# Performance work log

Measured on AMD Instinct MI355X. Metric: run time of the kernel, lower is better.

The kernel has to match this reference:

```python
import jax, jax.numpy as jnp
import numpy as np

D = 15            # tree depth; leaves at level 0, root at level D
INPUT_DIM = 64
MEM_DIM = 256     # must equal 4*INPUT_DIM (h-update mixes rr with x)
HID_DIM = 128


def _lin(key, fi, fo):
    kw, kb = jax.random.split(key)
    w = jax.random.normal(kw, (fi, fo), jnp.float32) / np.sqrt(fi)
    b = jax.random.normal(kb, (fo,), jnp.float32) * 0.01
    return w, b


def setup_inputs() -> dict:
    key = jax.random.key(0)
    N = 2 ** (D + 1) - 1          # 65535 nodes (complete binary tree, heap order)
    I = 2 ** D - 1                # internal nodes
    depth = np.floor(np.log2(np.arange(1, N + 1))).astype(np.int64)  # depth of node i
    node_order_np = D - depth     # leaves -> 0, root -> D
    parents = np.repeat(np.arange(I, dtype=np.int64), 2)   # sorted, consecutive per parent
    children = np.arange(1, N, dtype=np.int64)             # heap children 2i+1, 2i+2
    adjacency_list = jnp.asarray(np.stack([parents, children], axis=1))
    edge_order = jnp.asarray(node_order_np[parents])
    ks = jax.random.split(key, 24)
    inp = {
        'oper_feat': jax.random.uniform(ks[0], (N, 4), jnp.float32),
        'tb_feat': jax.random.uniform(ks[1], (N, 11), jnp.float32),
        'filter_feat': jax.random.uniform(ks[2], (N, 18), jnp.float32),
        'join_feat': jax.random.uniform(ks[3], (N, 37), jnp.float32),
        'c_a': jax.random.normal(ks[4], (N, MEM_DIM), jnp.float32) * 0.1,
        'c_b': jax.random.normal(ks[5], (N, 5 * INPUT_DIM), jnp.float32) * 0.1,
    }
    inp['w_op1'], inp['b_op1'] = _lin(ks[6], 4, INPUT_DIM)
    inp['w_op2'], inp['b_op2'] = _lin(ks[7], INPUT_DIM, INPUT_DIM)
    inp['w_tb1'], inp['b_tb1'] = _lin(ks[8], 11, INPUT_DIM)
    inp['w_tb2'], inp['b_tb2'] = _lin(ks[9], INPUT_DIM, INPUT_DIM)
    inp['w_ft1'], inp['b_ft1'] = _lin(ks[10], 18, INPUT_DIM)
    inp['w_ft2'], inp['b_ft2'] = _lin(ks[11], INPUT_DIM, INPUT_DIM)
    inp['w_jn1'], inp['b_jn1'] = _lin(ks[12], 37, INPUT_DIM)
    inp['w_jn2'], inp['b_jn2'] = _lin(ks[13], INPUT_DIM, INPUT_DIM)
    inp['w_xou'], inp['b_xou'] = _lin(ks[14], 4 * INPUT_DIM, 3 * MEM_DIM)
    inp['w_ab'], inp['b_ab'] = _lin(ks[15], MEM_DIM, MEM_DIM)
    inp['w_btoa'], inp['b_btoa'] = _lin(ks[16], 5 * INPUT_DIM, MEM_DIM)
    inp['w_ca'], inp['b_ca'] = _lin(ks[17], 4 * INPUT_DIM, MEM_DIM)
    inp['w_cb'], inp['b_cb'] = _lin(ks[18], 4 * INPUT_DIM, MEM_DIM)
    inp['w_o1'], inp['b_o1'] = _lin(ks[19], MEM_DIM, HID_DIM)
    inp['w_o2'], inp['b_o2'] = _lin(ks[20], HID_DIM, 1)
    inp['node_order'] = jnp.asarray(node_order_np)
    inp['adjacency_list'] = adjacency_list
    inp['edge_order'] = edge_order
    inp['feed'] = 0
    return inp


def _mlp2(f, w1, b1, w2, b2):
    return jax.nn.relu(jax.nn.relu(f @ w1 + b1) @ w2 + b2)


def reference(oper_feat, tb_feat, filter_feat, join_feat, c_a, c_b,
              w_op1, b_op1, w_op2, b_op2, w_tb1, b_tb1, w_tb2, b_tb2,
              w_ft1, b_ft1, w_ft2, b_ft2, w_jn1, b_jn1, w_jn2, b_jn2,
              w_xou, b_xou, w_ab, b_ab, w_btoa, b_btoa, w_ca, b_ca,
              w_cb, b_cb, w_o1, b_o1, w_o2, b_o2,
              node_order, adjacency_list, edge_order, feed):
    N = node_order.shape[0]
    op = _mlp2(oper_feat, w_op1, b_op1, w_op2, b_op2)
    tb = _mlp2(tb_feat, w_tb1, b_tb1, w_tb2, b_tb2)
    ft = _mlp2(filter_feat, w_ft1, b_ft1, w_ft2, b_ft2)
    jn = _mlp2(join_feat, w_jn1, b_jn1, w_jn2, b_jn2)
    x = jnp.concatenate([op, tb, ft, jn], axis=1)        # [N, 4*input_dim] == [N, mem_dim]
    xou = x @ w_xou + b_xou                               # [N, 3*mem_dim]
    xx, ff, rr = jnp.split(xou, 3, axis=1)
    ff = jax.nn.sigmoid(ff)
    rr = jax.nn.sigmoid(rr)
    cb = c_b @ w_btoa + b_btoa                            # con_mpl_btoa (no activation)
    wa = jax.nn.sigmoid(c_a @ w_ca + b_ca)
    wb = jax.nn.sigmoid(cb @ w_cb + b_cb)
    c_ab = jax.nn.relu((wa * c_a + wb * cb) @ w_ab + b_ab)
    c = jnp.zeros((N, MEM_DIM), x.dtype)
    h = jnp.zeros((N, MEM_DIM), x.dtype)
    c = jnp.where((node_order == 0)[:, None], c_a, c)
    c = jnp.where((node_order == feed)[:, None], c_ab, c)
    par = adjacency_list[:, 0]
    chi = adjacency_list[:, 1]
    L = int(node_order.max())
    for n in range(feed + 1, L + 1):
        em = (edge_order == n).astype(x.dtype)[:, None]
        # segment-sum children cell states into their parents (level-n edges only)
        c_sum = jax.ops.segment_sum(c[chi] * em, par, num_segments=N)
        nm = (node_order == n)[:, None]
        c = jnp.where(nm, ff * c_sum + (1.0 - ff) * xx, c)
        h = jnp.where(nm, rr * jnp.tanh(c) + (1.0 - rr) * x, h)
    hid = jax.nn.relu(h @ w_o1 + b_o1)
    return jax.nn.sigmoid(hid @ w_o2 + b_o2)              # [N, 1]
```

## Files before the change

kernel.cpp:

```cpp
#include <hip/hip_runtime.h>
#include <cstdint>

#define I_NODES 32767
#define N_NODES 65535
#define NLEAF   32768

typedef float f32x4 __attribute__((ext_vector_type(4)));
typedef short bf16x8 __attribute__((ext_vector_type(8)));
typedef int   i32x4 __attribute__((ext_vector_type(4)));

__device__ __forceinline__ float sigmoidf_(float v) {
    return 1.0f / (1.0f + __expf(-v));
}
__device__ __forceinline__ short f2bf(float f) {
    union { float f; unsigned u; } v; v.f = f;
    unsigned r = (v.u + 0x7FFF + ((v.u >> 16) & 1)) >> 16;
    return (short)r;
}
__device__ __forceinline__ float bf2f(short b) {
    union { float f; unsigned u; } v; v.u = ((unsigned)(unsigned short)b) << 16;
    return v.f;
}

__global__ __launch_bounds__(256) void encode_kernel(
    const float* __restrict__ oper, const float* __restrict__ tbf,
    const float* __restrict__ ftf,  const float* __restrict__ jnf,
    const float* __restrict__ w_op1, const float* __restrict__ b_op1,
    const float* __restrict__ w_op2, const float* __restrict__ b_op2,
    const float* __restrict__ w_tb1, const float* __restrict__ b_tb1,
    const float* __restrict__ w_tb2, const float* __restrict__ b_tb2,
    const float* __restrict__ w_ft1, const float* __restrict__ b_ft1,
    const float* __restrict__ w_ft2, const float* __restrict__ b_ft2,
    const float* __restrict__ w_jn1, const float* __restrict__ b_jn1,
    const float* __restrict__ w_jn2, const float* __restrict__ b_jn2,
    short* __restrict__ x_out)
{
    __shared__ float w1[70 * 64];
    __shared__ float w2s[64 * 64];
    __shared__ float b1[256], b2[256];
    __shared__ float feat[16][72];
    __shared__ float h1[16][256];

    const int tid = threadIdx.x;

    for (int idx = tid; idx < 70 * 64; idx += 256) {
        int r = idx >> 6, cc = idx & 63;
        float v;
        if (r < 4)       v = w_op1[r * 64 + cc];
        else if (r < 15) v = w_tb1[(r - 4) * 64 + cc];
        else if (r < 33) v = w_ft1[(r - 15) * 64 + cc];
        else             v = w_jn1[(r - 33) * 64 + cc];
        w1[idx] = v;
    }
    {
        int s = tid >> 6, jj = tid & 63;
        b1[tid] = (s == 0) ? b_op1[jj] : (s == 1) ? b_tb1[jj] : (s == 2) ? b_ft1[jj] : b_jn1[jj];
        b2[tid] = (s == 0) ? b_op2[jj] : (s == 1) ? b_tb2[jj] : (s == 2) ? b_ft2[jj] : b_jn2[jj];
    }

    const int node0 = blockIdx.x * 16;
    for (int idx = tid; idx < 16 * 70; idx += 256) {
        int nb = idx / 70, f = idx % 70;
        int node = node0 + nb;
        float v = 0.0f;
        if (node < I_NODES) {
            if (f < 4)       v = oper[node * 4 + f];
            else if (f < 15) v = tbf[node * 11 + (f - 4)];
            else if (f < 33) v = ftf[node * 18 + (f - 15)];
            else             v = jnf[node * 37 + (f - 33)];
        }
        feat[nb][f] = v;
    }
    __syncthreads();

    {
        int j = tid;
        int s = j >> 6, jj = j & 63;
        int off = (s == 0) ? 0 : (s == 1) ? 4 : (s == 2) ? 15 : 33;
        int Ks  = (s == 0) ? 4 : (s == 1) ? 11 : (s == 2) ? 18 : 37;
        for (int nb = 0; nb < 16; nb++) {
            float acc = b1[j];
            for (int k = 0; k < Ks; k++)
                acc += feat[nb][off + k] * w1[(off + k) * 64 + jj];
            h1[nb][j] = fmaxf(acc, 0.0f);
        }
    }
    __syncthreads();

    for (int s = 0; s < 4; s++) {
        const float* w2g = (s == 0) ? w_op2 : (s == 1) ? w_tb2 : (s == 2) ? w_ft2 : w_jn2;
        for (int idx = tid; idx < 4096; idx += 256) w2s[idx] = w2g[idx];
        __syncthreads();
        for (int it = 0; it < 4; it++) {
            int wi = it * 256 + tid;
            int nb = wi >> 6, jj = wi & 63;
            float acc = b2[s * 64 + jj];
            for (int k = 0; k < 64; k++)
                acc += h1[nb][s * 64 + k] * w2s[k * 64 + jj];
            int node = node0 + nb;
            x_out[(size_t)node * 256 + s * 64 + jj] =
                (node < I_NODES) ? f2bf(fmaxf(acc, 0.0f)) : (short)0;
        }
        __syncthreads();
    }
}

template <int ACT, int MODE>
__global__ __launch_bounds__(256) void gemm_mfma(
    const short* __restrict__ A, const short* __restrict__ Bt,
    const float* __restrict__ bias,
    float* __restrict__ fout0, float* __restrict__ fout1, float* __restrict__ fout2,
    short* __restrict__ bout,
    int M, int K, int Nn)
{
    __shared__ short Asl[128 * 40];
    __shared__ short Bsl[128 * 40];

    const int tid = threadIdx.x;
    const int bm = blockIdx.x * 128;
    const int bn = blockIdx.y * 128;
    const int wave = tid >> 6, lane = tid & 63;
    const int m = lane & 15, q = lane >> 4;
    const int rw = (wave & 1) * 64, cw = (wave >> 1) * 64;

    f32x4 acc[4][4] = {};

    for (int k0 = 0; k0 < K; k0 += 32) {
#pragma unroll
        for (int i = 0; i < 2; i++) {
            int id = tid + i * 256;
            int row = id >> 2, ch = id & 3;
            i32x4 va = *(const i32x4*)(A + (size_t)(bm + row) * K + k0 + ch * 8);
            *(i32x4*)&Asl[row * 40 + ch * 8] = va;
            i32x4 vb = *(const i32x4*)(Bt + (size_t)(bn + row) * K + k0 + ch * 8);
            *(i32x4*)&Bsl[row * 40 + ch * 8] = vb;
        }
        __syncthreads();

        bf16x8 bfrag[4];
#pragma unroll
        for (int ct = 0; ct < 4; ct++)
            bfrag[ct] = *(const bf16x8*)&Bsl[(cw + ct * 16 + m) * 40 + q * 8];
#pragma unroll
        for (int rt = 0; rt < 4; rt++) {
            bf16x8 afrag = *(const bf16x8*)&Asl[(rw + rt * 16 + m) * 40 + q * 8];
#pragma unroll
            for (int ct = 0; ct < 4; ct++)
                acc[rt][ct] = __builtin_amdgcn_mfma_f32_16x16x32_bf16(
                    afrag, bfrag[ct], acc[rt][ct], 0, 0, 0);
        }
        __syncthreads();
    }

#pragma unroll
    for (int rt = 0; rt < 4; rt++) {
#pragma unroll
        for (int ct = 0; ct < 4; ct++) {
            int col = bn + cw + ct * 16 + m;
            float bv = bias[col];
#pragma unroll
            for (int r = 0; r < 4; r++) {
                int row = bm + rw + rt * 16 + q * 4 + r;
                float v = acc[rt][ct][r] + bv;
                if (MODE == 0) {
                    if (ACT == 1) v = fmaxf(v, 0.0f);
                    else if (ACT == 2) v = sigmoidf_(v);
                    fout0[(size_t)row * Nn + col] = v;
                } else if (MODE == 1) {
                    int seg = col >> 8, cc = col & 255;
                    if (seg == 0)      fout0[(size_t)row * 256 + cc] = v;
                    else if (seg == 1) fout1[(size_t)row * 256 + cc] = sigmoidf_(v);
                    else               fout2[(size_t)row * 256 + cc] = sigmoidf_(v);
                } else {
                    if (ACT == 1) v = fmaxf(v, 0.0f);
                    else if (ACT == 2) v = sigmoidf_(v);
                    bout[(size_t)row * Nn + col] = f2bf(v);
                }
            }
        }
    }
}

__global__ __launch_bounds__(256) void convT_kernel(
    const float* __restrict__ w, short* __restrict__ o, int K, int Nn)
{
    int idx = blockIdx.x * 256 + threadIdx.x;
    if (idx >= K * Nn) return;
    int n = idx / K, k = idx - n * K;
    o[idx] = f2bf(w[(size_t)k * Nn + n]);
}

__global__ __launch_bounds__(256) void conv_leaf_kernel(
    const float* __restrict__ c_a, const float* __restrict__ c_b,
    short* __restrict__ ca_o, short* __restrict__ cb_o)
{
    size_t i = (size_t)blockIdx.x * 256 + threadIdx.x;
    if (i < (size_t)NLEAF * 256) ca_o[i] = f2bf(c_a[(size_t)I_NODES * 256 + i]);
    if (i < (size_t)NLEAF * 320) cb_o[i] = f2bf(c_b[(size_t)I_NODES * 320 + i]);
}

__global__ __launch_bounds__(256) void tcomb_kernel(
    short* __restrict__ wa, const short* __restrict__ wb,
    const short* __restrict__ cb, const float* __restrict__ c_a_leaf)
{
    size_t idx = (size_t)blockIdx.x * 256 + threadIdx.x;
    if (idx >= (size_t)NLEAF * 256) return;
    float v = bf2f(wa[idx]) * c_a_leaf[idx] + bf2f(wb[idx]) * bf2f(cb[idx]);
    wa[idx] = f2bf(v);
}

__global__ __launch_bounds__(256) void level_kernel(
    float* __restrict__ c, const float* __restrict__ ff,
    const float* __restrict__ xx, int start, int count)
{
    size_t idx = (size_t)blockIdx.x * 256 + threadIdx.x;
    if (idx >= (size_t)count * 256) return;
    int p = start + (int)(idx >> 8);
    int j = (int)(idx & 255);
    size_t pr = (size_t)p * 256 + j;
    float cs = c[(size_t)(2 * p + 1) * 256 + j] + c[(size_t)(2 * p + 2) * 256 + j];
    float f = ff[pr];
    c[pr] = f * cs + (1.0f - f) * xx[pr];
}

__global__ __launch_bounds__(256) void h_kernel(
    const float* __restrict__ c, const float* __restrict__ rr,
    const short* __restrict__ x, short* __restrict__ h)
{
    size_t idx = (size_t)blockIdx.x * 256 + threadIdx.x;
    int i = (int)(idx >> 8);
    if (i < I_NODES) {
        float r = rr[idx];
        h[idx] = f2bf(r * tanhf(c[idx]) + (1.0f - r) * bf2f(x[idx]));
    } else {
        h[idx] = 0;
    }
}

__global__ __launch_bounds__(256) void out2_kernel(
    const short* __restrict__ hid, const float* __restrict__ w_o2,
    const float* __restrict__ b_o2, float* __restrict__ out)
{
    int wave = threadIdx.x >> 6;
    int lane = threadIdx.x & 63;
    int node = blockIdx.x * 4 + wave;
    if (node >= N_NODES) return;
    const short* hrow = hid + (size_t)node * 128;
    float p = bf2f(hrow[lane]) * w_o2[lane] + bf2f(hrow[lane + 64]) * w_o2[lane + 64];
#pragma unroll
    for (int off = 32; off > 0; off >>= 1) p += __shfl_xor(p, off);
    if (lane == 0) out[node] = sigmoidf_(p + b_o2[0]);
}

extern "C" void kernel_launch(void* const* d_in, const int* in_sizes, int n_in,
                              void* d_out, int out_size, void* d_ws, size_t ws_size,
                              hipStream_t stream)
{
    const float* oper  = (const float*)d_in[0];
    const float* tbf   = (const float*)d_in[1];
    const float* ftf   = (const float*)d_in[2];
    const float* jnf   = (const float*)d_in[3];
    const float* c_a   = (const float*)d_in[4];
    const float* c_b   = (const float*)d_in[5];
    const float* w_op1 = (const float*)d_in[6],  *b_op1 = (const float*)d_in[7];
    const float* w_op2 = (const float*)d_in[8],  *b_op2 = (const float*)d_in[9];
    const float* w_tb1 = (const float*)d_in[10], *b_tb1 = (const float*)d_in[11];
    const float* w_tb2 = (const float*)d_in[12], *b_tb2 = (const float*)d_in[13];
    const float* w_ft1 = (const float*)d_in[14], *b_ft1 = (const float*)d_in[15];
    const float* w_ft2 = (const float*)d_in[16], *b_ft2 = (const float*)d_in[17];
    const float* w_jn1 = (const float*)d_in[18], *b_jn1 = (const float*)d_in[19];
    const float* w_jn2 = (const float*)d_in[20], *b_jn2 = (const float*)d_in[21];
    const float* w_xou = (const float*)d_in[22], *b_xou = (const float*)d_in[23];
    const float* w_ab  = (const float*)d_in[24], *b_ab  = (const float*)d_in[25];
    const float* w_btoa= (const float*)d_in[26], *b_btoa= (const float*)d_in[27];
    const float* w_ca  = (const float*)d_in[28], *b_ca  = (const float*)d_in[29];
    const float* w_cb  = (const float*)d_in[30], *b_cb  = (const float*)d_in[31];
    const float* w_o1  = (const float*)d_in[32], *b_o1  = (const float*)d_in[33];
    const float* w_o2  = (const float*)d_in[34], *b_o2  = (const float*)d_in[35];

    char* WS = (char*)d_ws;
    short* wT_xou  = (short*)WS;
    short* wT_btoa = wT_xou  + 768 * 256;
    short* wT_ca   = wT_btoa + 256 * 320;
    short* wT_cb   = wT_ca   + 256 * 256;
    short* wT_ab   = wT_cb   + 256 * 256;
    short* wT_o1   = wT_ab   + 256 * 256;
    const size_t OFF_X    = (size_t)1 << 20;
    const size_t OFF_XX   = OFF_X    + (size_t)32768 * 256 * 2;
    const size_t OFF_FF   = OFF_XX   + (size_t)32768 * 256 * 4;
    const size_t OFF_RR   = OFF_FF   + (size_t)32768 * 256 * 4;
    const size_t OFF_C    = OFF_RR   + (size_t)32768 * 256 * 4;
    const size_t OFF_CA   = OFF_C    + (size_t)65536 * 256 * 4;
    const size_t OFF_CBIN = OFF_CA   + (size_t)32768 * 256 * 2;
    const size_t OFF_CB   = OFF_CBIN + (size_t)32768 * 320 * 2;
    const size_t OFF_WA   = OFF_CB   + (size_t)32768 * 256 * 2;
    const size_t OFF_WB   = OFF_WA   + (size_t)32768 * 256 * 2;
    short* x    = (short*)(WS + OFF_X);
    float* xx   = (float*)(WS + OFF_XX);
    float* ff   = (float*)(WS + OFF_FF);
    float* rr   = (float*)(WS + OFF_RR);
    float* c    = (float*)(WS + OFF_C);
    short* cal  = (short*)(WS + OFF_CA);
    short* cbin = (short*)(WS + OFF_CBIN);
    short* cb   = (short*)(WS + OFF_CB);
    short* wa   = (short*)(WS + OFF_WA);
    short* wb   = (short*)(WS + OFF_WB);
    short* h    = (short*)(WS + OFF_CA);
    short* hid  = (short*)(WS + OFF_CB);
    float* out  = (float*)d_out;

    convT_kernel<<<(768 * 256 + 255) / 256, 256, 0, stream>>>(w_xou,  wT_xou,  256, 768);
    convT_kernel<<<(256 * 320 + 255) / 256, 256, 0, stream>>>(w_btoa, wT_btoa, 320, 256);
    convT_kernel<<<(256 * 256 + 255) / 256, 256, 0, stream>>>(w_ca,   wT_ca,   256, 256);
    convT_kernel<<<(256 * 256 + 255) / 256, 256, 0, stream>>>(w_cb,   wT_cb,   256, 256);
    convT_kernel<<<(256 * 256 + 255) / 256, 256, 0, stream>>>(w_ab,   wT_ab,   256, 256);
    convT_kernel<<<(128 * 256 + 255) / 256, 256, 0, stream>>>(w_o1,   wT_o1,   256, 128);
    conv_leaf_kernel<<<(NLEAF * 320 + 255) / 256, 256, 0, stream>>>(c_a, c_b, cal, cbin);

    encode_kernel<<<2048, 256, 0, stream>>>(
        oper, tbf, ftf, jnf,
        w_op1, b_op1, w_op2, b_op2, w_tb1, b_tb1, w_tb2, b_tb2,
        w_ft1, b_ft1, w_ft2, b_ft2, w_jn1, b_jn1, w_jn2, b_jn2, x);

    gemm_mfma<0, 1><<<dim3(256, 6), 256, 0, stream>>>(
        x, wT_xou, b_xou, xx, ff, rr, nullptr, 32768, 256, 768);

    gemm_mfma<0, 2><<<dim3(256, 2), 256, 0, stream>>>(
        cbin, wT_btoa, b_btoa, nullptr, nullptr, nullptr, cb, 32768, 320, 256);
    gemm_mfma<2, 2><<<dim3(256, 2), 256, 0, stream>>>(
        cal, wT_ca, b_ca, nullptr, nullptr, nullptr, wa, 32768, 256, 256);
    gemm_mfma<2, 2><<<dim3(256, 2), 256, 0, stream>>>(
        cb, wT_cb, b_cb, nullptr, nullptr, nullptr, wb, 32768, 256, 256);
    tcomb_kernel<<<NLEAF, 256, 0, stream>>>(wa, wb, cb, c_a + (size_t)I_NODES * 256);
    gemm_mfma<1, 0><<<dim3(256, 2), 256, 0, stream>>>(
        wa, wT_ab, b_ab, c + (size_t)I_NODES * 256, nullptr, nullptr, nullptr,
        32768, 256, 256);

    for (int n = 1; n <= 15; n++) {
        int d = 15 - n;
        int start = (1 << d) - 1;
        int count = 1 << d;
        level_kernel<<<count, 256, 0, stream>>>(c, ff, xx, start, count);
    }

    h_kernel<<<65536, 256, 0, stream>>>(c, rr, x, h);

    gemm_mfma<1, 2><<<dim3(512, 1), 256, 0, stream>>>(
        h, wT_o1, b_o1, nullptr, nullptr, nullptr, hid, 65536, 256, 128);
    out2_kernel<<<(N_NODES + 3) / 4, 256, 0, stream>>>(hid, w_o2, b_o2, out);
}
```

Measured before the change: 631.2 us.

## Restructure pipeline: MFMA encoder, fused gates, merged level/h kernels, leaf shortcut

The scalar encoder kernel becomes two bf16 MFMA GEMMs over packed, zero-padded features and block-diagonal weights. The six weight transposes are merged into one prep kernel, and the tcomb step is fused into the w_cb GEMM epilogue. The h computation is folded into the per-level kernel, and the eight smallest levels run in one single-block kernel to cut launch overhead. The output MLP now covers only internal nodes, and leaf outputs use relu(b_o1) because leaf h is zero. This brings extra bf16 rounding in the encoder, a fast tanh approximation, and a serial single-block tail.

After: 510.9 us. 1.24x faster.

```diff
diff --git a/kernel.cpp b/kernel.cpp
--- a/kernel.cpp
+++ b/kernel.cpp
@@ -11,6 +11,9 @@
 
 __device__ __forceinline__ float sigmoidf_(float v) {
     return 1.0f / (1.0f + __expf(-v));
+}
+__device__ __forceinline__ float tanhf_(float v) {
+    return 1.0f - 2.0f / (1.0f + __expf(2.0f * v));
 }
 __device__ __forceinline__ short f2bf(float f) {
     union { float f; unsigned u; } v; v.f = f;
@@ -22,95 +25,101 @@
     return v.f;
 }
 
-__global__ __launch_bounds__(256) void encode_kernel(
-    const float* __restrict__ oper, const float* __restrict__ tbf,
-    const float* __restrict__ ftf,  const float* __restrict__ jnf,
-    const float* __restrict__ w_op1, const float* __restrict__ b_op1,
-    const float* __restrict__ w_op2, const float* __restrict__ b_op2,
-    const float* __restrict__ w_tb1, const float* __restrict__ b_tb1,
-    const float* __restrict__ w_tb2, const float* __restrict__ b_tb2,
-    const float* __restrict__ w_ft1, const float* __restrict__ b_ft1,
-    const float* __restrict__ w_ft2, const float* __restrict__ b_ft2,
-    const float* __restrict__ w_jn1, const float* __restrict__ b_jn1,
-    const float* __restrict__ w_jn2, const float* __restrict__ b_jn2,
-    short* __restrict__ x_out)
-{
-    __shared__ float w1[70 * 64];
-    __shared__ float w2s[64 * 64];
-    __shared__ float b1[256], b2[256];
-    __shared__ float feat[16][72];
-    __shared__ float h1[16][256];
-
-    const int tid = threadIdx.x;
-
-    for (int idx = tid; idx < 70 * 64; idx += 256) {
-        int r = idx >> 6, cc = idx & 63;
-        float v;
-        if (r < 4)       v = w_op1[r * 64 + cc];
-        else if (r < 15) v = w_tb1[(r - 4) * 64 + cc];
-        else if (r < 33) v = w_ft1[(r - 15) * 64 + cc];
-        else             v = w_jn1[(r - 33) * 64 + cc];
-        w1[idx] = v;
-    }
-    {
-        int s = tid >> 6, jj = tid & 63;
-        b1[tid] = (s == 0) ? b_op1[jj] : (s == 1) ? b_tb1[jj] : (s == 2) ? b_ft1[jj] : b_jn1[jj];
-        b2[tid] = (s == 0) ? b_op2[jj] : (s == 1) ? b_tb2[jj] : (s == 2) ? b_ft2[jj] : b_jn2[jj];
-    }
-
-    const int node0 = blockIdx.x * 16;
-    for (int idx = tid; idx < 16 * 70; idx += 256) {
-        int nb = idx / 70, f = idx % 70;
-        int node = node0 + nb;
-        float v = 0.0f;
-        if (node < I_NODES) {
-            if (f < 4)       v = oper[node * 4 + f];
-            else if (f < 15) v = tbf[node * 11 + (f - 4)];
-            else if (f < 33) v = ftf[node * 18 + (f - 15)];
-            else             v = jnf[node * 37 + (f - 33)];
-        }
-        feat[nb][f] = v;
-    }
-    __syncthreads();
-
-    {
-        int j = tid;
+__global__ __launch_bounds__(256) void prep_weights(
+    const float* __restrict__ w_xou, const float* __restrict__ w_btoa,
+    const float* __restrict__ w_ca,  const float* __restrict__ w_cb,
+    const float* __restrict__ w_ab,  const float* __restrict__ w_o1,
+    const float* __restrict__ w_op1, const float* __restrict__ w_tb1,
+    const float* __restrict__ w_ft1, const float* __restrict__ w_jn1,
+    const float* __restrict__ w_op2, const float* __restrict__ w_tb2,
+    const float* __restrict__ w_ft2, const float* __restrict__ w_jn2,
+    const float* __restrict__ b_op1, const float* __restrict__ b_tb1,
+    const float* __restrict__ b_ft1, const float* __restrict__ b_jn1,
+    const float* __restrict__ b_op2, const float* __restrict__ b_tb2,
+    const float* __restrict__ b_ft2, const float* __restrict__ b_jn2,
+    short* __restrict__ wT_xou, short* __restrict__ wT_btoa,
+    short* __restrict__ wT_ca,  short* __restrict__ wT_cb,
+    short* __restrict__ wT_ab,  short* __restrict__ wT_o1,
+    short* __restrict__ W1T,    short* __restrict__ W2T,
+    float* __restrict__ b1cat,  float* __restrict__ b2cat)
+{
+    int r = blockIdx.x * 256 + threadIdx.x;
+    if (r < 196608) { wT_xou[r] = f2bf(w_xou[(size_t)(r % 256) * 768 + r / 256]); return; }
+    r -= 196608;
+    if (r < 81920)  { wT_btoa[r] = f2bf(w_btoa[(size_t)(r % 320) * 256 + r / 320]); return; }
+    r -= 81920;
+    if (r < 65536)  { wT_ca[r] = f2bf(w_ca[(size_t)(r % 256) * 256 + r / 256]); return; }
+    r -= 65536;
+    if (r < 65536)  { wT_cb[r] = f2bf(w_cb[(size_t)(r % 256) * 256 + r / 256]); return; }
+    r -= 65536;
+    if (r < 65536)  { wT_ab[r] = f2bf(w_ab[(size_t)(r % 256) * 256 + r / 256]); return; }
+    r -= 65536;
+    if (r < 32768)  { wT_o1[r] = f2bf(w_o1[(size_t)(r % 256) * 128 + r / 256]); return; }
+    r -= 32768;
+    if (r < 24576) {
+        int j = r / 96, k = r % 96;
         int s = j >> 6, jj = j & 63;
         int off = (s == 0) ? 0 : (s == 1) ? 4 : (s == 2) ? 15 : 33;
         int Ks  = (s == 0) ? 4 : (s == 1) ? 11 : (s == 2) ? 18 : 37;
-        for (int nb = 0; nb < 16; nb++) {
-            float acc = b1[j];
-            for (int k = 0; k < Ks; k++)
-                acc += feat[nb][off + k] * w1[(off + k) * 64 + jj];
-            h1[nb][j] = fmaxf(acc, 0.0f);
-        }
-    }
-    __syncthreads();
-
-    for (int s = 0; s < 4; s++) {
-        const float* w2g = (s == 0) ? w_op2 : (s == 1) ? w_tb2 : (s == 2) ? w_ft2 : w_jn2;
-        for (int idx = tid; idx < 4096; idx += 256) w2s[idx] = w2g[idx];
-        __syncthreads();
-        for (int it = 0; it < 4; it++) {
-            int wi = it * 256 + tid;
-            int nb = wi >> 6, jj = wi & 63;
-            float acc = b2[s * 64 + jj];
-            for (int k = 0; k < 64; k++)
-                acc += h1[nb][s * 64 + k] * w2s[k * 64 + jj];
-            int node = node0 + nb;
-            x_out[(size_t)node * 256 + s * 64 + jj] =
-                (node < I_NODES) ? f2bf(fmaxf(acc, 0.0f)) : (short)0;
-        }
-        __syncthreads();
-    }
+        const float* w = (s == 0) ? w_op1 : (s == 1) ? w_tb1 : (s == 2) ? w_ft1 : w_jn1;
+        W1T[r] = (k >= off && k < off + Ks) ? f2bf(w[(k - off) * 64 + jj]) : (short)0;
+        return;
+    }
+    r -= 24576;
+    if (r < 65536) {
+        int j = r >> 8, k = r & 255;
+        int s = j >> 6, jj = j & 63;
+        const float* w = (s == 0) ? w_op2 : (s == 1) ? w_tb2 : (s == 2) ? w_ft2 : w_jn2;
+        W2T[r] = ((k >> 6) == s) ? f2bf(w[(k & 63) * 64 + jj]) : (short)0;
+        return;
+    }
+    r -= 65536;
+    if (r < 256) {
+        int s = r >> 6, jj = r & 63;
+        b1cat[r] = (s == 0) ? b_op1[jj] : (s == 1) ? b_tb1[jj] : (s == 2) ? b_ft1[jj] : b_jn1[jj];
+        return;
+    }
+    r -= 256;
+    if (r < 256) {
+        int s = r >> 6, jj = r & 63;
+        b2cat[r] = (s == 0) ? b_op2[jj] : (s == 1) ? b_tb2[jj] : (s == 2) ? b_ft2[jj] : b_jn2[jj];
+    }
+}
+
+__global__ __launch_bounds__(256) void pack_feat(
+    const float* __restrict__ oper, const float* __restrict__ tbf,
+    const float* __restrict__ ftf,  const float* __restrict__ jnf,
+    short* __restrict__ xfeat)
+{
+    int idx = blockIdx.x * 256 + threadIdx.x;
+    int node = idx / 96, f = idx - node * 96;
+    float v = 0.0f;
+    if (node < I_NODES) {
+        if (f < 4)       v = oper[node * 4 + f];
+        else if (f < 15) v = tbf[node * 11 + (f - 4)];
+        else if (f < 33) v = ftf[node * 18 + (f - 15)];
+        else if (f < 70) v = jnf[node * 37 + (f - 33)];
+    }
+    xfeat[idx] = f2bf(v);
+}
+
+__global__ __launch_bounds__(256) void conv_leaf_kernel(
+    const float* __restrict__ c_a, const float* __restrict__ c_b,
+    short* __restrict__ ca_o, short* __restrict__ cb_o)
+{
+    size_t i = (size_t)blockIdx.x * 256 + threadIdx.x;
+    if (i < (size_t)NLEAF * 256) ca_o[i] = f2bf(c_a[(size_t)I_NODES * 256 + i]);
+    if (i < (size_t)NLEAF * 320) cb_o[i] = f2bf(c_b[(size_t)I_NODES * 320 + i]);
 }
 
 template <int ACT, int MODE>
 __global__ __launch_bounds__(256) void gemm_mfma(
     const short* __restrict__ A, const short* __restrict__ Bt,
     const float* __restrict__ bias,
-    float* __restrict__ fout0, float* __restrict__ fout1, float* __restrict__ fout2,
+    float* __restrict__ fout0, const float* __restrict__ caf,
+    float* __restrict__ fout1, float* __restrict__ fout2,
     short* __restrict__ bout,
+    const short* __restrict__ e1, const short* __restrict__ e2,
     int M, int K, int Nn)
 {
     __shared__ short Asl[128 * 40];
@@ -171,82 +180,80 @@
                     if (seg == 0)      fout0[(size_t)row * 256 + cc] = v;
                     else if (seg == 1) fout1[(size_t)row * 256 + cc] = sigmoidf_(v);
                     else               fout2[(size_t)row * 256 + cc] = sigmoidf_(v);
-                } else {
+                } else if (MODE == 2) {
                     if (ACT == 1) v = fmaxf(v, 0.0f);
                     else if (ACT == 2) v = sigmoidf_(v);
                     bout[(size_t)row * Nn + col] = f2bf(v);
+                } else {
+                    size_t idx = (size_t)row * 256 + col;
+                    float t = bf2f(e1[idx]) * caf[idx] + sigmoidf_(v) * bf2f(e2[idx]);
+                    bout[idx] = f2bf(t);
                 }
             }
         }
     }
 }
 
-__global__ __launch_bounds__(256) void convT_kernel(
-    const float* __restrict__ w, short* __restrict__ o, int K, int Nn)
-{
-    int idx = blockIdx.x * 256 + threadIdx.x;
-    if (idx >= K * Nn) return;
-    int n = idx / K, k = idx - n * K;
-    o[idx] = f2bf(w[(size_t)k * Nn + n]);
-}
-
-__global__ __launch_bounds__(256) void conv_leaf_kernel(
-    const float* __restrict__ c_a, const float* __restrict__ c_b,
-    short* __restrict__ ca_o, short* __restrict__ cb_o)
-{
-    size_t i = (size_t)blockIdx.x * 256 + threadIdx.x;
-    if (i < (size_t)NLEAF * 256) ca_o[i] = f2bf(c_a[(size_t)I_NODES * 256 + i]);
-    if (i < (size_t)NLEAF * 320) cb_o[i] = f2bf(c_b[(size_t)I_NODES * 320 + i]);
-}
-
-__global__ __launch_bounds__(256) void tcomb_kernel(
-    short* __restrict__ wa, const short* __restrict__ wb,
-    const short* __restrict__ cb, const float* __restrict__ c_a_leaf)
-{
-    size_t idx = (size_t)blockIdx.x * 256 + threadIdx.x;
-    if (idx >= (size_t)NLEAF * 256) return;
-    float v = bf2f(wa[idx]) * c_a_leaf[idx] + bf2f(wb[idx]) * bf2f(cb[idx]);
-    wa[idx] = f2bf(v);
-}
-
 __global__ __launch_bounds__(256) void level_kernel(
     float* __restrict__ c, const float* __restrict__ ff,
-    const float* __restrict__ xx, int start, int count)
+    const float* __restrict__ xx, const float* __restrict__ rr,
+    const short* __restrict__ x, short* __restrict__ h,
+    int start)
 {
     size_t idx = (size_t)blockIdx.x * 256 + threadIdx.x;
-    if (idx >= (size_t)count * 256) return;
     int p = start + (int)(idx >> 8);
     int j = (int)(idx & 255);
     size_t pr = (size_t)p * 256 + j;
     float cs = c[(size_t)(2 * p + 1) * 256 + j] + c[(size_t)(2 * p + 2) * 256 + j];
     float f = ff[pr];
-    c[pr] = f * cs + (1.0f - f) * xx[pr];
-}
-
-__global__ __launch_bounds__(256) void h_kernel(
-    const float* __restrict__ c, const float* __restrict__ rr,
+    float cv = f * cs + (1.0f - f) * xx[pr];
+    c[pr] = cv;
+    float r = rr[pr];
+    h[pr] = f2bf(r * tanhf_(cv) + (1.0f - r) * bf2f(x[pr]));
+}
+
+__global__ __launch_bounds__(1024) void small_levels_kernel(
+    float* __restrict__ c, const float* __restrict__ ff,
+    const float* __restrict__ xx, const float* __restrict__ rr,
     const short* __restrict__ x, short* __restrict__ h)
 {
-    size_t idx = (size_t)blockIdx.x * 256 + threadIdx.x;
-    int i = (int)(idx >> 8);
-    if (i < I_NODES) {
-        float r = rr[idx];
-        h[idx] = f2bf(r * tanhf(c[idx]) + (1.0f - r) * bf2f(x[idx]));
-    } else {
-        h[idx] = 0;
+    const int tid = threadIdx.x;
+    for (int n = 8; n <= 15; n++) {
+        int d = 15 - n;
+        int start = (1 << d) - 1;
+        int total = (1 << d) * 256;
+        for (int idx = tid; idx < total; idx += 1024) {
+            int p = start + (idx >> 8);
+            int j = idx & 255;
+            size_t pr = (size_t)p * 256 + j;
+            float cs = c[(size_t)(2 * p + 1) * 256 + j] + c[(size_t)(2 * p + 2) * 256 + j];
+            float f = ff[pr];
+            float cv = f * cs + (1.0f - f) * xx[pr];
+            c[pr] = cv;
+            float r = rr[pr];
+            h[pr] = f2bf(r * tanhf_(cv) + (1.0f - r) * bf2f(x[pr]));
+        }
+        __syncthreads();
     }
 }
 
 __global__ __launch_bounds__(256) void out2_kernel(
     const short* __restrict__ hid, const float* __restrict__ w_o2,
-    const float* __restrict__ b_o2, float* __restrict__ out)
+    const float* __restrict__ b_o2, const float* __restrict__ b_o1,
+    float* __restrict__ out)
 {
     int wave = threadIdx.x >> 6;
     int lane = threadIdx.x & 63;
     int node = blockIdx.x * 4 + wave;
     if (node >= N_NODES) return;
-    const short* hrow = hid + (size_t)node * 128;
-    float p = bf2f(hrow[lane]) * w_o2[lane] + bf2f(hrow[lane + 64]) * w_o2[lane + 64];
+    float h0, h1;
+    if (node < I_NODES) {
+        const short* hrow = hid + (size_t)node * 128;
+        h0 = bf2f(hrow[lane]); h1 = bf2f(hrow[lane + 64]);
+    } else {
+        h0 = fmaxf(b_o1[lane], 0.0f); h1 = fmaxf(b_o1[lane + 64], 0.0f);
+    }
+    float p = h0 * w_o2[lane] + h1 * w_o2[lane + 64];
 #pragma unroll
     for (int off = 32; off > 0; off >>= 1) p += __shfl_xor(p, off);
     if (lane == 0) out[node] = sigmoidf_(p + b_o2[0]);
@@ -280,12 +287,19 @@
 
     char* WS = (char*)d_ws;
     short* wT_xou  = (short*)WS;
-    short* wT_btoa = wT_xou  + 768 * 256;
-    short* wT_ca   = wT_btoa + 256 * 320;
-    short* wT_cb   = wT_ca   + 256 * 256;
-    short* wT_ab   = wT_cb   + 256 * 256;
-    short* wT_o1   = wT_ab   + 256 * 256;
-    const size_t OFF_X    = (size_t)1 << 20;
+    short* wT_btoa = wT_xou  + 196608;
+    short* wT_ca   = wT_btoa + 81920;
+    short* wT_cb   = wT_ca   + 65536;
+    short* wT_ab   = wT_cb   + 65536;
+    short* wT_o1   = wT_ab   + 65536;
+    short* W1T     = wT_o1   + 32768;
+    short* W2T     = W1T     + 24576;
+    float* b1cat   = (float*)(W2T + 65536);
+    float* b2cat   = b1cat + 256;
+    const size_t MB = 1 << 20;
+    const size_t OFF_XF   = 2 * MB;
+    const size_t OFF_HE   = OFF_XF   + (size_t)32768 * 96 * 2;
+    const size_t OFF_X    = OFF_HE   + (size_t)32768 * 256 * 2;
     const size_t OFF_XX   = OFF_X    + (size_t)32768 * 256 * 2;
     const size_t OFF_FF   = OFF_XX   + (size_t)32768 * 256 * 4;
     const size_t OFF_RR   = OFF_FF   + (size_t)32768 * 256 * 4;
@@ -294,58 +308,65 @@
     const size_t OFF_CBIN = OFF_CA   + (size_t)32768 * 256 * 2;
     const size_t OFF_CB   = OFF_CBIN + (size_t)32768 * 320 * 2;
     const size_t OFF_WA   = OFF_CB   + (size_t)32768 * 256 * 2;
-    const size_t OFF_WB   = OFF_WA   + (size_t)32768 * 256 * 2;
-    short* x    = (short*)(WS + OFF_X);
-    float* xx   = (float*)(WS + OFF_XX);
-    float* ff   = (float*)(WS + OFF_FF);
-    float* rr   = (float*)(WS + OFF_RR);
-    float* c    = (float*)(WS + OFF_C);
-    short* cal  = (short*)(WS + OFF_CA);
-    short* cbin = (short*)(WS + OFF_CBIN);
-    short* cb   = (short*)(WS + OFF_CB);
-    short* wa   = (short*)(WS + OFF_WA);
-    short* wb   = (short*)(WS + OFF_WB);
-    short* h    = (short*)(WS + OFF_CA);
-    short* hid  = (short*)(WS + OFF_CB);
-    float* out  = (float*)d_out;
-
-    convT_kernel<<<(768 * 256 + 255) / 256, 256, 0, stream>>>(w_xou,  wT_xou,  256, 768);
-    convT_kernel<<<(256 * 320 + 255) / 256, 256, 0, stream>>>(w_btoa, wT_btoa, 320, 256);
-    convT_kernel<<<(256 * 256 + 255) / 256, 256, 0, stream>>>(w_ca,   wT_ca,   256, 256);
-    convT_kernel<<<(256 * 256 + 255) / 256, 256, 0, stream>>>(w_cb,   wT_cb,   256, 256);
-    convT_kernel<<<(256 * 256 + 255) / 256, 256, 0, stream>>>(w_ab,   wT_ab,   256, 256);
-    convT_kernel<<<(128 * 256 + 255) / 256, 256, 0, stream>>>(w_o1,   wT_o1,   256, 128);
+
+    short* xfeat = (short*)(WS + OFF_XF);
+    short* henc  = (short*)(WS + OFF_HE);
+    short* x     = (short*)(WS + OFF_X);
+    float* xx    = (float*)(WS + OFF_XX);
+    float* ff    = (float*)(WS + OFF_FF);
+    float* rr    = (float*)(WS + OFF_RR);
+    float* c     = (float*)(WS + OFF_C);
+    short* cal   = (short*)(WS + OFF_CA);
+    short* cbin  = (short*)(WS + OFF_CBIN);
+    short* cb    = (short*)(WS + OFF_CB);
+    short* wa    = (short*)(WS + OFF_WA);
+    short* h     = (short*)(WS + OFF_CA);
+    short* hid   = (short*)(WS + OFF_CB);
+    float* out   = (float*)d_out;
+    const float* caf = c_a + (size_t)I_NODES * 256;
+
+    prep_weights<<<(598528 + 255) / 256, 256, 0, stream>>>(
+        w_xou, w_btoa, w_ca, w_cb, w_ab, w_o1,
+        w_op1, w_tb1, w_ft1, w_jn1, w_op2, w_tb2, w_ft2, w_jn2,
+        b_op1, b_tb1, b_ft1, b_jn1, b_op2, b_tb2, b_ft2, b_jn2,
+        wT_xou, wT_btoa, wT_ca, wT_cb, wT_ab, wT_o1, W1T, W2T, b1cat, b2cat);
+    pack_feat<<<(32768 * 96) / 256, 256, 0, stream>>>(oper, tbf, ftf, jnf, xfeat);
     conv_leaf_kernel<<<(NLEAF * 320 + 255) / 256, 256, 0, stream>>>(c_a, c_b, cal, cbin);
 
-    encode_kernel<<<2048, 256, 0, stream>>>(
-        oper, tbf, ftf, jnf,
-        w_op1, b_op1, w_op2, b_op2, w_tb1, b_tb1, w_tb2, b_tb2,
-        w_ft1, b_ft1, w_ft2, b_ft2, w_jn1, b_jn1, w_jn2, b_jn2, x);
+    gemm_mfma<1, 2><<<dim3(256, 2), 256, 0, stream>>>(
+        xfeat, W1T, b1cat, nullptr, nullptr, nullptr, nullptr, henc, nullptr, nullptr,
+        32768, 96, 256);
+    gemm_mfma<1, 2><<<dim3(256, 2), 256, 0, stream>>>(
+        henc, W2T, b2cat, nullptr, nullptr, nullptr, nullptr, x, nullptr, nullptr,
+        32768, 256, 256);
 
     gemm_mfma<0, 1><<<dim3(256, 6), 256, 0, stream>>>(
-        x, wT_xou, b_xou, xx, ff, rr, nullptr, 32768, 256, 768);
+        x, wT_xou, b_xou, xx, nullptr, ff, rr, nullptr, nullptr, nullptr,
+        32768, 256, 768);
 
     gemm_mfma<0, 2><<<dim3(256, 2), 256, 0, stream>>>(
-        cbin, wT_btoa, b_btoa, nullptr, nullptr, nullptr, cb, 32768, 320, 256);
+        cbin, wT_btoa, b_btoa, nullptr, nullptr, nullptr, nullptr, cb, nullptr, nullptr,
+        32768, 320, 256);
     gemm_mfma<2, 2><<<dim3(256, 2), 256, 0, stream>>>(
-        cal, wT_ca, b_ca, nullptr, nullptr, nullptr, wa, 32768, 256, 256);
-    gemm_mfma<2, 2><<<dim3(256, 2), 256, 0, stream>>>(
-        cb, wT_cb, b_cb, nullptr, nullptr, nullptr, wb, 32768, 256, 256);
-    tcomb_kernel<<<NLEAF, 256, 0, stream>>>(wa, wb, cb, c_a + (size_t)I_NODES * 256);
+        cal, wT_ca, b_ca, nullptr, nullptr, nullptr, nullptr, wa, nullptr, nullptr,
+        32768, 256, 256);
+    gemm_mfma<0, 3><<<dim3(256, 2), 256, 0, stream>>>(
+        cb, wT_cb, b_cb, nullptr, caf, nullptr, nullptr, wa , wa, cb,
+        32768, 256, 256);
     gemm_mfma<1, 0><<<dim3(256, 2), 256, 0, stream>>>(
         wa, wT_ab, b_ab, c + (size_t)I_NODES * 256, nullptr, nullptr, nullptr,
-        32768, 256, 256);
-
-    for (int n = 1; n <= 15; n++) {
+        nullptr, nullptr, nullptr, 32768, 256, 256);
+
+    for (int n = 1; n <= 7; n++) {
         int d = 15 - n;
         int start = (1 << d) - 1;
         int count = 1 << d;
-        level_kernel<<<count, 256, 0, stream>>>(c, ff, xx, start, count);
-    }
-
-    h_kernel<<<65536, 256, 0, stream>>>(c, rr, x, h);
-
-    gemm_mfma<1, 2><<<dim3(512, 1), 256, 0, stream>>>(
-        h, wT_o1, b_o1, nullptr, nullptr, nullptr, hid, 65536, 256, 128);
-    out2_kernel<<<(N_NODES + 3) / 4, 256, 0, stream>>>(hid, w_o2, b_o2, out);
-}
+        level_kernel<<<count, 256, 0, stream>>>(c, ff, xx, rr, x, h, start);
+    }
+    small_levels_kernel<<<1, 1024, 0, stream>>>(c, ff, xx, rr, x, h);
+
+    gemm_mfma<1, 2><<<dim3(256, 1), 256, 0, stream>>>(
+        h, wT_o1, b_o1, nullptr, nullptr, nullptr, nullptr, hid, nullptr, nullptr,
+        32768, 256, 128);
+    out2_kernel<<<(N_NODES + 3) / 4, 256, 0, stream>>>(hid, w_o2, b_o2, b_o1, out);
+}
```
